# Kernel optimization log

Hardware: AMD Instinct MI355X
Metric: run time of the kernel (lower is better)

The kernel has to match this reference:

```python
import jax, jax.numpy as jnp
import numpy as np

D_MODEL = 1024
NUM_HEADS = 16
HEAD_DIM = D_MODEL // NUM_HEADS


def setup_inputs() -> dict:
    key = jax.random.key(0)
    ks = jax.random.split(key, 7)
    B, S = 4, 2048
    scale = 1.0 / np.sqrt(D_MODEL)
    x = jax.random.normal(ks[0], (B, S, D_MODEL), dtype=jnp.float32)
    Wq = jax.random.normal(ks[1], (D_MODEL, D_MODEL), dtype=jnp.float32) * scale
    Wk = jax.random.normal(ks[2], (D_MODEL, D_MODEL), dtype=jnp.float32) * scale
    Wv = jax.random.normal(ks[3], (D_MODEL, D_MODEL), dtype=jnp.float32) * scale
    bq = jax.random.normal(ks[4], (D_MODEL,), dtype=jnp.float32) * 0.02
    bk = jax.random.normal(ks[5], (D_MODEL,), dtype=jnp.float32) * 0.02
    bv = jax.random.normal(ks[6], (D_MODEL,), dtype=jnp.float32) * 0.02
    return {"x": x, "Wq": Wq, "bq": bq, "Wk": Wk, "bk": bk, "Wv": Wv, "bv": bv}


def reference(x, Wq, bq, Wk, bk, Wv, bv):
    B, S, _ = x.shape
    # QKV projections (nn.Linear: x @ W^T + b; here W stored as [in, out] already)
    q = x @ Wq + bq
    k = x @ Wk + bk
    v = x @ Wv + bv
    # [B, H, S, Dh]
    def split_heads(t):
        return t.reshape(B, S, NUM_HEADS, HEAD_DIM).transpose(0, 2, 1, 3)
    q, k, v = split_heads(q), split_heads(k), split_heads(v)
    # NOTE: module scales by sqrt(d_model), NOT sqrt(head_dim)
    scores = jnp.einsum("bhqd,bhkd->bhqk", q, k) / jnp.sqrt(jnp.float32(D_MODEL))
    attn = jax.nn.softmax(scores, axis=-1)  # dropout = identity (eval mode)
    out = jnp.einsum("bhqk,bhkd->bhqd", attn, v)
    return out.transpose(0, 2, 1, 3).reshape(B, S, D_MODEL)
```

## Files before the change

kernel.cpp:

```cpp
#include <hip/hip_runtime.h>


typedef __attribute__((ext_vector_type(8))) __bf16 bf16x8;
typedef __attribute__((ext_vector_type(8))) unsigned short ushort8;
typedef __attribute__((ext_vector_type(4))) float floatx4;

#if __has_builtin(__builtin_amdgcn_exp2f)
#define EXP2(x) __builtin_amdgcn_exp2f(x)
#else
#define EXP2(x) __expf((x) * 0.6931471805599453f)
#endif

__device__ __forceinline__ unsigned short f2bf(float f) {
    __bf16 h = (__bf16)f;
    return __builtin_bit_cast(unsigned short, h);
}
__device__ __forceinline__ bf16x8 pack8(floatx4 a, floatx4 b) {
    bf16x8 v = {(__bf16)a[0], (__bf16)a[1], (__bf16)a[2], (__bf16)a[3],
                (__bf16)b[0], (__bf16)b[1], (__bf16)b[2], (__bf16)b[3]};
    return v;
}
__device__ __forceinline__ floatx4 mfma16(bf16x8 a, bf16x8 b, floatx4 c) {
    return __builtin_amdgcn_mfma_f32_16x16x32_bf16(a, b, c, 0, 0, 0);
}
__device__ __forceinline__ int spos(int s) {
    int rk = s & 31;
    return (s & ~31) | (((rk & 15) >> 2) * 8 + ((rk >> 4) << 2) + (rk & 3));
}
__device__ __forceinline__ void glds16(const void* g, void* l) {
    __builtin_amdgcn_global_load_lds(
        (const __attribute__((address_space(1))) unsigned int*)g,
        (__attribute__((address_space(3))) unsigned int*)l, 16, 0, 0);
}

__global__ __launch_bounds__(256) void prep_x(const float* __restrict__ X,
                                              unsigned short* __restrict__ Xb) {
    int i = (blockIdx.x * 256 + threadIdx.x) * 8;
    float4 a = *(const float4*)&X[i];
    float4 b = *(const float4*)&X[i + 4];
    bf16x8 v = {(__bf16)a.x, (__bf16)a.y, (__bf16)a.z, (__bf16)a.w,
                (__bf16)b.x, (__bf16)b.y, (__bf16)b.z, (__bf16)b.w};
    *(bf16x8*)&Xb[i] = v;
}

__global__ __launch_bounds__(256) void prep_wt(
    const float* __restrict__ Wq, const float* __restrict__ Wk,
    const float* __restrict__ Wv,
    unsigned short* __restrict__ WqT, unsigned short* __restrict__ WkT,
    unsigned short* __restrict__ WvT) {
    __shared__ unsigned short Ls[64 * 72];
    const int tid = threadIdx.x, z = blockIdx.z;
    const float* W = (z == 0) ? Wq : (z == 1) ? Wk : Wv;
    unsigned short* WT = (z == 0) ? WqT : (z == 1) ? WkT : WvT;
    const int k0 = (blockIdx.x >> 4) * 64, o0 = (blockIdx.x & 15) * 64;
#pragma unroll
    for (int e = 0; e < 4; ++e) {
        int idx = e * 256 + tid;
        int r = idx >> 4, c = (idx & 15) * 4;
        float4 f = *(const float4*)&W[(size_t)(k0 + r) * 1024 + o0 + c];
        Ls[(c + 0) * 72 + r] = f2bf(f.x);
        Ls[(c + 1) * 72 + r] = f2bf(f.y);
        Ls[(c + 2) * 72 + r] = f2bf(f.z);
        Ls[(c + 3) * 72 + r] = f2bf(f.w);
    }
    __syncthreads();
#pragma unroll
    for (int e = 0; e < 2; ++e) {
        int idx = e * 256 + tid;
        int rr = idx >> 3, ch = (idx & 7) * 8;
        *(ushort8*)&WT[(size_t)(o0 + rr) * 1024 + k0 + ch] =
            *(const ushort8*)&Ls[rr * 72 + ch];
    }
}

__global__ __launch_bounds__(256, 3) void qkv_gemm(
    const unsigned short* __restrict__ Xb,
    const unsigned short* __restrict__ WqT,
    const unsigned short* __restrict__ WkT,
    const unsigned short* __restrict__ WvT,
    const float* __restrict__ bq, const float* __restrict__ bk,
    const float* __restrict__ bv,
    unsigned short* __restrict__ Kh, unsigned short* __restrict__ Vt,
    float* __restrict__ Qs_out) {

    __shared__ __align__(16) unsigned char arena[32768];

    const int tid = threadIdx.x;
    const int w = tid >> 6, lane = tid & 63;
    const int l15 = lane & 15, quad = lane >> 4;
    const int z = blockIdx.z;
    const int tok_base = blockIdx.x * 128, o_base = blockIdx.y * 128;
    const int wr = w >> 1, wc = w & 1;

    const unsigned short* Wsrc = (z == 0) ? WkT : (z == 1) ? WvT : WqT;
    const char* Asrc = (z == 1) ? (const char*)(Wsrc + (size_t)o_base * 1024)
                                : (const char*)(Xb + (size_t)tok_base * 1024);
    const char* Bsrc = (z == 1) ? (const char*)(Xb + (size_t)tok_base * 1024)
                                : (const char*)(Wsrc + (size_t)o_base * 1024);

    const int coff = (((lane & 7) ^ (lane >> 3)) << 4);
    const char* pa[4];
    const char* pb[4];
    unsigned char* la[4];
    unsigned char* lb[4];
#pragma unroll
    for (int e = 0; e < 4; ++e) {
        int r = (e * 4 + w) * 8 + (lane >> 3);
        pa[e] = Asrc + (size_t)r * 2048 + coff;
        pb[e] = Bsrc + (size_t)r * 2048 + coff;
        la[e] = arena + (e * 4 + w) * 1024;
        lb[e] = arena + 16384 + (e * 4 + w) * 1024;
    }

    const unsigned cq = (unsigned)((quad ^ (l15 & 7)) << 4);
    unsigned offA[4], offB[4];
#pragma unroll
    for (int t = 0; t < 4; ++t) {
        offA[t] = (unsigned)((wr * 64 + t * 16 + l15) * 128) + cq;
        offB[t] = 16384u + (unsigned)((wc * 64 + t * 16 + l15) * 128) + cq;
    }

    floatx4 acc[4][4];
#pragma unroll
    for (int mt = 0; mt < 4; ++mt)
#pragma unroll
        for (int nt = 0; nt < 4; ++nt) acc[mt][nt] = (floatx4){0.f, 0.f, 0.f, 0.f};

    for (int k0 = 0; k0 < 1024; k0 += 64) {
        __syncthreads();
#pragma unroll
        for (int e = 0; e < 4; ++e) {
            glds16(pa[e], la[e]);
            glds16(pb[e], lb[e]);
            pa[e] += 128;
            pb[e] += 128;
        }
        __syncthreads();

#pragma unroll
        for (int kc = 0; kc < 2; ++kc) {
            bf16x8 af[4], bfr[4];
#pragma unroll
            for (int mt = 0; mt < 4; ++mt)
                af[mt] = *(const bf16x8*)&arena[offA[mt] ^ (unsigned)(kc << 6)];
#pragma unroll
            for (int nt = 0; nt < 4; ++nt)
                bfr[nt] = *(const bf16x8*)&arena[offB[nt] ^ (unsigned)(kc << 6)];
#pragma unroll
            for (int mt = 0; mt < 4; ++mt)
#pragma unroll
                for (int nt = 0; nt < 4; ++nt)
                    acc[mt][nt] = mfma16(af[mt], bfr[nt], acc[mt][nt]);
        }
    }

    if (z == 0) {
#pragma unroll
        for (int nt = 0; nt < 4; ++nt) {
            int col = o_base + wc * 64 + nt * 16 + l15;
            float bia = bk[col];
            int h = col >> 6, dh = col & 63;
#pragma unroll
            for (int mt = 0; mt < 4; ++mt)
#pragma unroll
                for (int r = 0; r < 4; ++r) {
                    int t = tok_base + wr * 64 + mt * 16 + quad * 4 + r;
                    int bb = t >> 11, s = t & 2047;
                    Kh[(((size_t)(bb * 16 + h)) * 2048 + s) * 64 + dh] =
                        f2bf(acc[mt][nt][r] + bia);
                }
        }
    } else if (z == 1) {
#pragma unroll
        for (int mt = 0; mt < 4; ++mt)
#pragma unroll
            for (int r = 0; r < 4; ++r) {
                int o = o_base + wr * 64 + mt * 16 + quad * 4 + r;
                float bia = bv[o];
#pragma unroll
                for (int nt = 0; nt < 4; ++nt) {
                    int t = tok_base + wc * 64 + nt * 16 + l15;
                    int bb = t >> 11, s = t & 2047;
                    Vt[((size_t)(bb * 1024 + o)) * 2048 + spos(s)] =
                        f2bf(acc[mt][nt][r] + bia);
                }
            }
    } else {
        const float QS = 0.03125f * 1.44269504f;
#pragma unroll
        for (int nt = 0; nt < 4; ++nt) {
            int col = o_base + wc * 64 + nt * 16 + l15;
            float bia = bq[col];
#pragma unroll
            for (int mt = 0; mt < 4; ++mt)
#pragma unroll
                for (int r = 0; r < 4; ++r) {
                    int t = tok_base + wr * 64 + mt * 16 + quad * 4 + r;
                    Qs_out[(size_t)t * 1024 + col] = (acc[mt][nt][r] + bia) * QS;
                }
        }
    }
}

__global__ __launch_bounds__(256, 4) void attn_kernel(
    const unsigned short* __restrict__ Kh,
    const unsigned short* __restrict__ Vt,
    float* __restrict__ out) {

    __shared__ __align__(16) unsigned char arena[32768];

    const int tid = threadIdx.x;
    const int w = tid >> 6, lane = tid & 63;
    const int l15 = lane & 15, quad = lane >> 4;
    const int qb = blockIdx.x, h = blockIdx.y, b = blockIdx.z;
    const size_t head_elems = ((size_t)(b * 16 + h)) * 2048 * 64;

    bf16x8 aq[2][2];
#pragma unroll
    for (int g = 0; g < 2; ++g)
#pragma unroll
        for (int kc = 0; kc < 2; ++kc) {
            const float* qp = out +
                (size_t)(b * 2048 + qb * 128 + w * 32 + g * 16 + l15) * 1024 +
                h * 64 + kc * 32 + quad * 8;
            floatx4 x0 = *(const floatx4*)qp;
            floatx4 x1 = *(const floatx4*)(qp + 4);
            aq[g][kc] = pack8(x0, x1);
        }
    __builtin_amdgcn_sched_barrier(0);

    const int coff = (((lane & 7) ^ (lane >> 3)) << 4);
    const char* pk[2];
    const char* pv[2];
    unsigned char* lk[2];
    unsigned char* lv[2];
#pragma unroll
    for (int e = 0; e < 2; ++e) {
        int r = (e * 4 + w) * 8 + (lane >> 3);
        pk[e] = (const char*)Kh + head_elems * 2 + (size_t)r * 128 + coff;
        pv[e] = (const char*)Vt + ((size_t)(b * 1024 + h * 64 + r)) * 4096 + coff;
        lk[e] = arena + (e * 4 + w) * 1024;
        lv[e] = arena + 8192 + (e * 4 + w) * 1024;
    }
    auto stage = [&](int bufsel) {
        int bo = bufsel << 14;
#pragma unroll
        for (int e = 0; e < 2; ++e) {
            glds16(pk[e], lk[e] + bo);
            glds16(pv[e], lv[e] + bo);
            pk[e] += 8192;
            pv[e] += 128;
        }
    };

    unsigned kb[4], vb[4];
#pragma unroll
    for (int t = 0; t < 4; ++t) {
        int rk = t * 16 + l15;
        unsigned sw = (unsigned)((quad ^ (rk & 7)) << 4);
        kb[t] = (unsigned)(rk * 128) + sw;
        vb[t] = 8192u + (unsigned)(rk * 128) + sw;
    }

    float l_part[2] = {0.f, 0.f};
    floatx4 O[2][4];
#pragma unroll
    for (int g = 0; g < 2; ++g)
#pragma unroll
        for (int n4 = 0; n4 < 4; ++n4) O[g][n4] = (floatx4){0.f, 0.f, 0.f, 0.f};

    stage(0);

#pragma unroll 1
    for (int kt = 0; kt < 32; ++kt) {
        if (kt < 31) {
            stage((kt + 1) & 1);
            asm volatile("s_waitcnt vmcnt(4)" ::: "memory");
        } else {
            asm volatile("s_waitcnt vmcnt(0)" ::: "memory");
        }
        __builtin_amdgcn_s_barrier();
        const unsigned bsel = (unsigned)((kt & 1) << 14);

        bf16x8 ap[2][2];
#pragma unroll
        for (int kg = 0; kg < 2; ++kg) {
            floatx4 s0[2], s1[2];
#pragma unroll
            for (int mm = 0; mm < 2; ++mm) {
                int m16 = 2 * kg + mm;
                unsigned ka = kb[m16] ^ bsel;
                bf16x8 kf0 = *(const bf16x8*)&arena[ka];
                bf16x8 kf1 = *(const bf16x8*)&arena[ka ^ 64u];
#pragma unroll
                for (int g = 0; g < 2; ++g) {
                    floatx4 a0 = (floatx4){0.f, 0.f, 0.f, 0.f};
                    a0 = mfma16(kf0, aq[g][0], a0);
                    a0 = mfma16(kf1, aq[g][1], a0);
                    if (mm == 0) s0[g] = a0; else s1[g] = a0;
                }
            }
#pragma unroll
            for (int g = 0; g < 2; ++g) {
                floatx4 p0, p1;
#pragma unroll
                for (int r = 0; r < 4; ++r) {
                    p0[r] = EXP2(fminf(s0[g][r], 43.28f));
                    p1[r] = EXP2(fminf(s1[g][r], 43.28f));
                }
                l_part[g] += (p0[0] + p0[1]) + (p0[2] + p0[3]) +
                             (p1[0] + p1[1]) + (p1[2] + p1[3]);
                ap[g][kg] = pack8(p0, p1);
            }
        }

#pragma unroll
        for (int n4 = 0; n4 < 4; ++n4)
#pragma unroll
            for (int kg = 0; kg < 2; ++kg) {
                bf16x8 vf = *(const bf16x8*)
                    &arena[(vb[n4] ^ bsel) ^ (unsigned)(kg << 6)];
#pragma unroll
                for (int g = 0; g < 2; ++g)
                    O[g][n4] = mfma16(ap[g][kg], vf, O[g][n4]);
            }

        asm volatile("s_waitcnt lgkmcnt(0)" ::: "memory");
        __builtin_amdgcn_s_barrier();
    }

#pragma unroll
    for (int g = 0; g < 2; ++g) {
        float l = l_part[g];
        l += __shfl_xor(l, 16);
        l += __shfl_xor(l, 32);
#pragma unroll
        for (int r = 0; r < 4; ++r) {
            float lr = __shfl(l, (lane & 48) | (quad * 4 + r));
            float inv = 1.f / lr;
            int srow = qb * 128 + w * 32 + g * 16 + quad * 4 + r;
#pragma unroll
            for (int n4 = 0; n4 < 4; ++n4)
                out[((size_t)(b * 2048 + srow)) * 1024 + h * 64 + n4 * 16 + l15] =
                    O[g][n4][r] * inv;
        }
    }
}

extern "C" void kernel_launch(void* const* d_in, const int* in_sizes, int n_in,
                              void* d_out, int out_size, void* d_ws, size_t ws_size,
                              hipStream_t stream) {
    const float *x, *Wq, *bq, *Wk, *bk, *Wv, *bv;
    x = (const float*)d_in[0];
    if (in_sizes[2] == 1024) {
        Wq = (const float*)d_in[1];  bq = (const float*)d_in[2];
        Wk = (const float*)d_in[3];  bk = (const float*)d_in[4];
        Wv = (const float*)d_in[5];  bv = (const float*)d_in[6];
    } else {
        Wq = (const float*)d_in[1];  Wk = (const float*)d_in[2];
        Wv = (const float*)d_in[3];
        bq = (const float*)d_in[4];  bk = (const float*)d_in[5];
        bv = (const float*)d_in[6];
    }
    float* out = (float*)d_out;

    char* ws = (char*)d_ws;
    unsigned short* Xb  = (unsigned short*)(ws);
    unsigned short* Kh  = (unsigned short*)(ws + (16u << 20));
    unsigned short* Vt  = (unsigned short*)(ws + (32u << 20));
    unsigned short* WqT = (unsigned short*)(ws + (48u << 20));
    unsigned short* WkT = (unsigned short*)(ws + (50u << 20));
    unsigned short* WvT = (unsigned short*)(ws + (52u << 20));

    prep_x<<<4096, 256, 0, stream>>>(x, Xb);
    prep_wt<<<dim3(256, 1, 3), 256, 0, stream>>>(Wq, Wk, Wv, WqT, WkT, WvT);
    qkv_gemm<<<dim3(64, 8, 3), 256, 0, stream>>>(Xb, WqT, WkT, WvT, bq, bk, bv,
                                                 Kh, Vt, out);
    attn_kernel<<<dim3(16, 16, 4), 256, 0, stream>>>(Kh, Vt, out);
}
```

Measured before the change: 232.0 us.

## Double-buffer QKV GEMM LDS loads, compute softmax row sums via MFMA, add setprio

The QKV projection GEMM now double-buffers its LDS tiles (64KB arena, occupancy hint lowered from 3 to 2). The next K-slice's global-to-LDS copy is issued before computing on the current one, replacing the two-syncthreads-per-iteration pattern. In attention, the per-row softmax denominators are accumulated by an MFMA against a ones vector instead of scalar adds plus cross-lane shuffles. The fminf clamp before exp2 is removed, and s_setprio brackets the MFMA sections. Dropping the clamp risks overflow for large scores, and the doubled LDS reduces occupancy.

```diff
diff --git a/kernel.cpp b/kernel.cpp
--- a/kernel.cpp
+++ b/kernel.cpp
@@ -73,7 +73,7 @@
     }
 }
 
-__global__ __launch_bounds__(256, 3) void qkv_gemm(
+__global__ __launch_bounds__(256, 2) void qkv_gemm(
     const unsigned short* __restrict__ Xb,
     const unsigned short* __restrict__ WqT,
     const unsigned short* __restrict__ WkT,
@@ -83,7 +83,7 @@
     unsigned short* __restrict__ Kh, unsigned short* __restrict__ Vt,
     float* __restrict__ Qs_out) {
 
-    __shared__ __align__(16) unsigned char arena[32768];
+    __shared__ __align__(16) unsigned char arena[65536];
 
     const int tid = threadIdx.x;
     const int w = tid >> 6, lane = tid & 63;
@@ -111,6 +111,16 @@
         la[e] = arena + (e * 4 + w) * 1024;
         lb[e] = arena + 16384 + (e * 4 + w) * 1024;
     }
+    auto stage = [&](int t) {
+        int bo = (t & 1) << 15;
+#pragma unroll
+        for (int e = 0; e < 4; ++e) {
+            glds16(pa[e], la[e] + bo);
+            glds16(pb[e], lb[e] + bo);
+            pa[e] += 128;
+            pb[e] += 128;
+        }
+    };
 
     const unsigned cq = (unsigned)((quad ^ (l15 & 7)) << 4);
     unsigned offA[4], offB[4];
@@ -126,32 +136,41 @@
 #pragma unroll
         for (int nt = 0; nt < 4; ++nt) acc[mt][nt] = (floatx4){0.f, 0.f, 0.f, 0.f};
 
-    for (int k0 = 0; k0 < 1024; k0 += 64) {
-        __syncthreads();
-#pragma unroll
-        for (int e = 0; e < 4; ++e) {
-            glds16(pa[e], la[e]);
-            glds16(pb[e], lb[e]);
-            pa[e] += 128;
-            pb[e] += 128;
-        }
-        __syncthreads();
-
+    stage(0);
+
+#pragma unroll 1
+    for (int t = 0; t < 16; ++t) {
+        if (t < 15) {
+            stage(t + 1);
+            asm volatile("s_waitcnt vmcnt(8)" ::: "memory");
+        } else {
+            asm volatile("s_waitcnt vmcnt(0)" ::: "memory");
+        }
+        __builtin_amdgcn_s_barrier();
+        const unsigned bsel = (unsigned)((t & 1) << 15);
+
+        __builtin_amdgcn_s_setprio(1);
 #pragma unroll
         for (int kc = 0; kc < 2; ++kc) {
             bf16x8 af[4], bfr[4];
 #pragma unroll
             for (int mt = 0; mt < 4; ++mt)
-                af[mt] = *(const bf16x8*)&arena[offA[mt] ^ (unsigned)(kc << 6)];
+                af[mt] = *(const bf16x8*)
+                    &arena[(offA[mt] ^ (unsigned)(kc << 6)) ^ bsel];
 #pragma unroll
             for (int nt = 0; nt < 4; ++nt)
-                bfr[nt] = *(const bf16x8*)&arena[offB[nt] ^ (unsigned)(kc << 6)];
+                bfr[nt] = *(const bf16x8*)
+                    &arena[(offB[nt] ^ (unsigned)(kc << 6)) ^ bsel];
 #pragma unroll
             for (int mt = 0; mt < 4; ++mt)
 #pragma unroll
                 for (int nt = 0; nt < 4; ++nt)
                     acc[mt][nt] = mfma16(af[mt], bfr[nt], acc[mt][nt]);
         }
+        __builtin_amdgcn_s_setprio(0);
+
+        asm volatile("s_waitcnt lgkmcnt(0)" ::: "memory");
+        __builtin_amdgcn_s_barrier();
     }
 
     if (z == 0) {
@@ -262,12 +281,16 @@
         vb[t] = 8192u + (unsigned)(rk * 128) + sw;
     }
 
-    float l_part[2] = {0.f, 0.f};
+    const bf16x8 ONES = {(__bf16)1.f, (__bf16)1.f, (__bf16)1.f, (__bf16)1.f,
+                         (__bf16)1.f, (__bf16)1.f, (__bf16)1.f, (__bf16)1.f};
+    floatx4 lacc[2];
     floatx4 O[2][4];
 #pragma unroll
-    for (int g = 0; g < 2; ++g)
+    for (int g = 0; g < 2; ++g) {
+        lacc[g] = (floatx4){0.f, 0.f, 0.f, 0.f};
 #pragma unroll
         for (int n4 = 0; n4 < 4; ++n4) O[g][n4] = (floatx4){0.f, 0.f, 0.f, 0.f};
+    }
 
     stage(0);
 
@@ -286,6 +309,7 @@
 #pragma unroll
         for (int kg = 0; kg < 2; ++kg) {
             floatx4 s0[2], s1[2];
+            __builtin_amdgcn_s_setprio(1);
 #pragma unroll
             for (int mm = 0; mm < 2; ++mm) {
                 int m16 = 2 * kg + mm;
@@ -300,20 +324,21 @@
                     if (mm == 0) s0[g] = a0; else s1[g] = a0;
                 }
             }
+            __builtin_amdgcn_s_setprio(0);
 #pragma unroll
             for (int g = 0; g < 2; ++g) {
                 floatx4 p0, p1;
 #pragma unroll
                 for (int r = 0; r < 4; ++r) {
-                    p0[r] = EXP2(fminf(s0[g][r], 43.28f));
-                    p1[r] = EXP2(fminf(s1[g][r], 43.28f));
+                    p0[r] = EXP2(s0[g][r]);
+                    p1[r] = EXP2(s1[g][r]);
                 }
-                l_part[g] += (p0[0] + p0[1]) + (p0[2] + p0[3]) +
-                             (p1[0] + p1[1]) + (p1[2] + p1[3]);
                 ap[g][kg] = pack8(p0, p1);
+                lacc[g] = mfma16(ap[g][kg], ONES, lacc[g]);
             }
         }
 
+        __builtin_amdgcn_s_setprio(1);
 #pragma unroll
         for (int n4 = 0; n4 < 4; ++n4)
 #pragma unroll
@@ -324,27 +349,23 @@
                 for (int g = 0; g < 2; ++g)
                     O[g][n4] = mfma16(ap[g][kg], vf, O[g][n4]);
             }
+        __builtin_amdgcn_s_setprio(0);
 
         asm volatile("s_waitcnt lgkmcnt(0)" ::: "memory");
         __builtin_amdgcn_s_barrier();
     }
 
 #pragma unroll
-    for (int g = 0; g < 2; ++g) {
-        float l = l_part[g];
-        l += __shfl_xor(l, 16);
-        l += __shfl_xor(l, 32);
+    for (int g = 0; g < 2; ++g)
 #pragma unroll
         for (int r = 0; r < 4; ++r) {
-            float lr = __shfl(l, (lane & 48) | (quad * 4 + r));
-            float inv = 1.f / lr;
+            float inv = 1.f / lacc[g][r];
             int srow = qb * 128 + w * 32 + g * 16 + quad * 4 + r;
 #pragma unroll
             for (int n4 = 0; n4 < 4; ++n4)
                 out[((size_t)(b * 2048 + srow)) * 1024 + h * 64 + n4 * 16 + l15] =
                     O[g][n4][r] * inv;
         }
-    }
 }
 
 extern "C" void kernel_launch(void* const* d_in, const int* in_sizes, int n_in,
```

New measurement: 225.4 us. 2.9% less time.
